# Performance work log

Measured on AMD Instinct MI355X. Metric: run time of the kernel, lower is better.

## Reference

```python
import jax, jax.numpy as jnp
import numpy as np

GAMMAK = 1.0 / 256.0  # 1/(2*d) so kernel values don't underflow for unit-gaussian data


def setup_inputs() -> dict:
    key = jax.random.key(0)
    k1, k2, k3, k4, k5 = jax.random.split(key, 5)
    N, d = 8192, 128
    X = jax.random.normal(k1, (N, d), dtype=jnp.float32)
    y = jax.random.normal(k2, (N - 1, d), dtype=jnp.float32)
    y_next = jax.random.normal(k3, (N - 1, d), dtype=jnp.float32)
    # reset_transform initializes R=eye, t=0; perturb slightly for nontrivial math
    R = jnp.eye(d, dtype=jnp.float32) + 0.01 * jax.random.normal(k4, (d, d), dtype=jnp.float32)
    t = 0.01 * jax.random.normal(k5, (d, 1), dtype=jnp.float32)
    return {"X": X, "y": y, "y_next": y_next, "R": R, "t": t}


def reference(X, y, y_next, R, t):
    # _transform_pts: (R @ y.T + t).T == y @ R.T + t.squeeze()
    yt = y @ R.T + t[:, 0]            # (N-1, d)
    Xb = X[:-1]                        # (N-1, d) kernel base points
    # pairwise_sqeuclidean(Xb, yt), clamped at 0
    sq = jnp.clip(
        jnp.sum(Xb * Xb, axis=1)[:, None]
        + jnp.sum(yt * yt, axis=1)[None, :]
        - 2.0 * (Xb @ yt.T),
        0.0, None,
    )                                  # (N-1, N-1)
    G = jnp.exp(-GAMMAK * sq)
    # diag(1/rowsum) @ G  ==  G / rowsum[:, None]  (avoids explicit NxN diagonal)
    y_pred = (G / jnp.sum(G, axis=1, keepdims=True)) @ X[1:]  # (N-1, d)
    return y_pred
```

## Files before the change

kernel.cpp:

```cpp
#include <hip/hip_runtime.h>


#define LOG2E 1.44269504088896340736f
#define KNEG (-(1.0f/256.0f)*LOG2E)
#define KA2C (2.0f*(1.0f/256.0f)*LOG2E)

typedef __attribute__((ext_vector_type(4)))  float f32x4;
typedef __attribute__((ext_vector_type(16))) float f32x16;
typedef __attribute__((ext_vector_type(8)))  short bf16x8;
typedef __attribute__((ext_vector_type(4)))  short bf16x4;

#if __has_builtin(__builtin_amdgcn_mfma_f32_32x32x8bf16_1k)
#define PV_DIRECT 1
#else
#define PV_DIRECT 0
#endif

__device__ __forceinline__ unsigned short f2bf(float f) {
  unsigned u = __builtin_bit_cast(unsigned, f);
  u = (u + 0x7fffu + ((u >> 16) & 1u)) >> 16;
  return (unsigned short)u;
}
__device__ __forceinline__ unsigned pk2bf(float a, float b) {
  return (unsigned)f2bf(a) | ((unsigned)f2bf(b) << 16);
}
__device__ __forceinline__ float fast_exp2(float x) {
#if __has_builtin(__builtin_amdgcn_exp2f)
  return __builtin_amdgcn_exp2f(x);
#else
  return exp2f(x);
#endif
}
__device__ __forceinline__ void gl2lds16(const void* g, void* l) {
  __builtin_amdgcn_global_load_lds((const __attribute__((address_space(1))) unsigned int*)g,
                                   (__attribute__((address_space(3))) unsigned int*)l, 16, 0, 0);
}
__device__ __forceinline__ void gl2lds4(const void* g, void* l) {
  __builtin_amdgcn_global_load_lds((const __attribute__((address_space(1))) unsigned int*)g,
                                   (__attribute__((address_space(3))) unsigned int*)l, 4, 0, 0);
}
__device__ __forceinline__ f32x16 mfma_32x32x16(bf16x8 a, bf16x8 b, f32x16 c) {
  return __builtin_amdgcn_mfma_f32_32x32x16_bf16(a, b, c, 0, 0, 0);
}
#if PV_DIRECT
__device__ __forceinline__ f32x16 mfma_32x32x8(bf16x4 a, bf16x4 b, f32x16 c) {
  return __builtin_amdgcn_mfma_f32_32x32x8bf16_1k(a, b, c, 0, 0, 0);
}
#endif

__global__ __launch_bounds__(128) void k_yt(const float* __restrict__ y,
                                            const float* __restrict__ R,
                                            const float* __restrict__ t,
                                            unsigned short* __restrict__ ytp,
                                            float* __restrict__ ynp) {
  __shared__ unsigned short ytt[64 * 132];
  const int tid = threadIdx.x;
  const int wv = tid >> 6;
  const int ln = tid & 63;
  const int l = ln & 31, h = ln >> 5;
  const int T = blockIdx.x;
  const int rw = T * 64 + wv * 32;

  bf16x8 af[8];
  {
    int row = rw + l; if (row > 8190) row = 8190;
    const float* yr = y + (size_t)row * 128;
#pragma unroll
    for (int kc = 0; kc < 8; ++kc) {
      float4 p0 = *(const float4*)(yr + kc*16 + 8*h);
      float4 p1 = *(const float4*)(yr + kc*16 + 8*h + 4);
      bf16x8 v;
      v[0]=(short)f2bf(p0.x); v[1]=(short)f2bf(p0.y); v[2]=(short)f2bf(p0.z); v[3]=(short)f2bf(p0.w);
      v[4]=(short)f2bf(p1.x); v[5]=(short)f2bf(p1.y); v[6]=(short)f2bf(p1.z); v[7]=(short)f2bf(p1.w);
      af[kc] = v;
    }
  }
  f32x16 acc[4];
#pragma unroll
  for (int cc=0; cc<4; ++cc)
#pragma unroll
    for (int i=0;i<16;++i) acc[cc][i] = 0.f;
#pragma unroll
  for (int cc=0; cc<4; ++cc) {
    const float* Rr = R + (size_t)(cc*32 + l) * 128;
#pragma unroll
    for (int kc=0; kc<8; ++kc) {
      float4 p0 = *(const float4*)(Rr + kc*16 + 8*h);
      float4 p1 = *(const float4*)(Rr + kc*16 + 8*h + 4);
      bf16x8 b;
      b[0]=(short)f2bf(p0.x); b[1]=(short)f2bf(p0.y); b[2]=(short)f2bf(p0.z); b[3]=(short)f2bf(p0.w);
      b[4]=(short)f2bf(p1.x); b[5]=(short)f2bf(p1.y); b[6]=(short)f2bf(p1.z); b[7]=(short)f2bf(p1.w);
      acc[cc] = mfma_32x32x16(af[kc], b, acc[cc]);
    }
  }
  float tv0 = t[l], tv1 = t[32+l], tv2 = t[64+l], tv3 = t[96+l];
  float v0[16], v1[16], v2[16], v3[16], ssq[16];
#pragma unroll
  for (int r=0;r<16;++r) {
    v0[r]=acc[0][r]+tv0; v1[r]=acc[1][r]+tv1; v2[r]=acc[2][r]+tv2; v3[r]=acc[3][r]+tv3;
    ssq[r] = v0[r]*v0[r] + v1[r]*v1[r] + v2[r]*v2[r] + v3[r]*v3[r];
  }
#pragma unroll
  for (int off=1; off<32; off<<=1)
#pragma unroll
    for (int r=0;r<16;++r) ssq[r] += __shfl_xor(ssq[r], off, 64);
  if (l < 16) {
    int r = l;
    int row = rw + (r&3) + 8*(r>>2) + 4*h;
    float val = KNEG * ssq[r];
    if (row >= 8191) val = -1e30f;
    ynp[row] = val;
  }
#pragma unroll
  for (int r=0;r<16;++r) {
    int rloc = wv*32 + (r&3) + 8*(r>>2) + 4*h;
    ytt[rloc*132 +   0 + l] = f2bf(v0[r]);
    ytt[rloc*132 +  32 + l] = f2bf(v1[r]);
    ytt[rloc*132 +  64 + l] = f2bf(v2[r]);
    ytt[rloc*132 +  96 + l] = f2bf(v3[r]);
  }
  __syncthreads();
#pragma unroll
  for (int kc=0;kc<8;++kc) {
    const unsigned short* s = &ytt[(wv*32 + l)*132 + kc*16 + 8*h];
    uint2 a = *(const uint2*)(s);
    uint2 b = *(const uint2*)(s + 4);
    uint4 o; o.x=a.x; o.y=a.y; o.z=b.x; o.w=b.y;
    *(uint4*)(ytp + (size_t)T*8192 + wv*4096 + kc*512 + ln*8) = o;
  }
}

__global__ __launch_bounds__(256) void k_x(const float* __restrict__ X,
                                           unsigned short* __restrict__ x1tp,
                                           float* __restrict__ xnp) {
  __shared__ float xt[65 * 132];
  __shared__ float ps[64][4];
  const int tid = threadIdx.x;
  const int T = blockIdx.x;
  const int jt = T * 64;
  {
    int rr = tid >> 2, q4 = tid & 3;
    int row = jt + rr; if (row > 8191) row = 8191;
    const float* src = X + (size_t)row*128 + q4*32;
    float* dst = &xt[rr*132 + q4*32];
    float s = 0.f;
#pragma unroll
    for (int i=0;i<8;++i) {
      float4 p = *(const float4*)(src + i*4);
      s += p.x*p.x + p.y*p.y + p.z*p.z + p.w*p.w;
      *(float4*)(dst + i*4) = p;
    }
    ps[rr][q4] = s;
    if (tid < 4) {
      int row2 = jt + 64; if (row2 > 8191) row2 = 8191;
      const float* s2 = X + (size_t)row2*128 + tid*32;
      float* d2 = &xt[64*132 + tid*32];
#pragma unroll
      for (int i=0;i<8;++i) *(float4*)(d2 + i*4) = *(const float4*)(s2 + i*4);
    }
  }
  __syncthreads();
  if (tid < 64) xnp[jt + tid] = KNEG * (ps[tid][0] + ps[tid][1] + ps[tid][2] + ps[tid][3]);
#if PV_DIRECT
#pragma unroll
  for (int it=0; it<8; ++it) {
    int E = tid + it*256;
    int lp = E & 63, grp = E >> 6;
    int cc = grp & 3, s = (grp >> 2) & 3, jc = grp >> 4;
    int jb = jc*32 + s*8 + 4*(lp>>5);
    int c  = cc*32 + (lp & 31);
    uint2 o;
    o.x = pk2bf(xt[(jb+1)*132 + c], xt[(jb+2)*132 + c]);
    o.y = pk2bf(xt[(jb+3)*132 + c], xt[(jb+4)*132 + c]);
    *(uint2*)(x1tp + (size_t)T*8192 + E*4) = o;
  }
#else
#pragma unroll
  for (int it=0; it<4; ++it) {
    int E = tid + it*256;
    int lp = E & 63, grp = E >> 6;
    int cc = grp & 3, jc16 = grp >> 2;
    int jb = jc16*16 + 8*(lp>>5);
    int c  = cc*32 + (lp & 31);
    uint4 o;
    o.x = pk2bf(xt[(jb+1)*132 + c], xt[(jb+2)*132 + c]);
    o.y = pk2bf(xt[(jb+3)*132 + c], xt[(jb+4)*132 + c]);
    o.z = pk2bf(xt[(jb+5)*132 + c], xt[(jb+6)*132 + c]);
    o.w = pk2bf(xt[(jb+7)*132 + c], xt[(jb+8)*132 + c]);
    *(uint4*)(x1tp + (size_t)T*8192 + E*8) = o;
  }
#endif
}

__global__ __launch_bounds__(256, 2) void k_main(
    const float* __restrict__ X,
    const unsigned short* __restrict__ ytp,
    const unsigned short* __restrict__ x1tp,
    const float* __restrict__ xnp,
    const float* __restrict__ ynp,
    float* __restrict__ accp,
    float* __restrict__ rsp,
    int tps) {
  __shared__ unsigned short yts[8192];
  __shared__ unsigned short vts[8192];
  __shared__ float yns[64];
#if !PV_DIRECT
  __shared__ unsigned short gls[4*32*68];
#endif
  const int tid = threadIdx.x;
  const int wv = tid >> 6, ln = tid & 63;
  const int l = ln & 31, h = ln >> 5;
  const int row = blockIdx.x*128 + wv*32 + l;

  bf16x8 qf[8];
  {
    const float* xr = X + (size_t)row * 128;
#pragma unroll
    for (int kc=0;kc<8;++kc) {
      float4 p0 = *(const float4*)(xr + kc*16 + 8*h);
      float4 p1 = *(const float4*)(xr + kc*16 + 8*h + 4);
      bf16x8 v;
      v[0]=(short)f2bf(p0.x); v[1]=(short)f2bf(p0.y); v[2]=(short)f2bf(p0.z); v[3]=(short)f2bf(p0.w);
      v[4]=(short)f2bf(p1.x); v[5]=(short)f2bf(p1.y); v[6]=(short)f2bf(p1.z); v[7]=(short)f2bf(p1.w);
      qf[kc]=v;
    }
  }
  const float xnl = xnp[row];
  f32x16 acc[4];
#pragma unroll
  for (int cc=0;cc<4;++cc)
#pragma unroll
    for (int i=0;i<16;++i) acc[cc][i]=0.f;
  float rs = 0.f;
  const int T0 = blockIdx.y * tps;
  for (int T = T0; T < T0 + tps; ++T) {
    __syncthreads();
    {
      const char* yb = (const char*)(ytp + (size_t)T*8192);
      const char* vb = (const char*)(x1tp + (size_t)T*8192);
#pragma unroll
      for (int i=0;i<4;++i) {
        int off = (wv*4 + i) * 1024;
        gl2lds16(yb + off + ln*16, (char*)yts + off);
        gl2lds16(vb + off + ln*16, (char*)vts + off);
      }
      if (wv == 0) gl2lds4(ynp + T*64 + ln, (char*)yns);
    }
    __syncthreads();
#pragma unroll
    for (int jc=0; jc<2; ++jc) {
      f32x16 sa;
#pragma unroll
      for (int i=0;i<16;++i) sa[i]=0.f;
#pragma unroll
      for (int kc=0;kc<8;++kc) {
        bf16x8 a = *(const bf16x8*)((const char*)yts + (jc*8+kc)*1024 + ln*16);
        sa = mfma_32x32x16(a, qf[kc], sa);
      }
      float gg[16];
#pragma unroll
      for (int rg=0; rg<4; ++rg) {
        f32x4 yv = *(const f32x4*)((const char*)yns + (jc*32 + rg*8 + 4*h)*4);
#pragma unroll
        for (int i=0;i<4;++i) {
          float e = fmaf(sa[rg*4+i], KA2C, xnl + yv[i]);
          e = fminf(e, 0.f);
          float g = fast_exp2(e);
          gg[rg*4+i] = g;
          rs += g;
        }
      }
#if PV_DIRECT
      bf16x4 pf[4];
#pragma unroll
      for (int s=0;s<4;++s) {
        bf16x4 p;
        p[0]=(short)f2bf(gg[4*s+0]); p[1]=(short)f2bf(gg[4*s+1]);
        p[2]=(short)f2bf(gg[4*s+2]); p[3]=(short)f2bf(gg[4*s+3]);
        pf[s]=p;
      }
#pragma unroll
      for (int s=0;s<4;++s)
#pragma unroll
        for (int cc=0;cc<4;++cc) {
          bf16x4 a = *(const bf16x4*)((const char*)vts + ((jc*16 + s*4 + cc)*512) + ln*8);
          acc[cc] = mfma_32x32x8(a, pf[s], acc[cc]);
        }
#else
#pragma unroll
      for (int p=0;p<8;++p) {
        int j0 = jc*32 + 2*(p&1) + 8*(p>>1) + 4*h;
        *(unsigned*)&gls[(wv*32 + l)*68 + j0] = pk2bf(gg[2*p], gg[2*p+1]);
      }
      __builtin_amdgcn_wave_barrier();
#pragma unroll
      for (int jj=0; jj<2; ++jj) {
        int jc16 = jc*2 + jj;
        const unsigned short* gp = &gls[(wv*32 + l)*68 + jc16*16 + 8*h];
        uint2 g0 = *(const uint2*)(gp);
        uint2 g1 = *(const uint2*)(gp + 4);
        uint4 gv; gv.x=g0.x; gv.y=g0.y; gv.z=g1.x; gv.w=g1.y;
        bf16x8 pb = __builtin_bit_cast(bf16x8, gv);
#pragma unroll
        for (int cc=0;cc<4;++cc) {
          bf16x8 a2 = *(const bf16x8*)((const char*)vts + (jc16*4+cc)*1024 + ln*16);
          acc[cc] = mfma_32x32x16(a2, pb, acc[cc]);
        }
      }
      __builtin_amdgcn_wave_barrier();
#endif
    }
  }
  rs += __shfl_xor(rs, 32, 64);
  const int sp = blockIdx.y;
  if (h == 0) rsp[(size_t)sp*8192 + row] = rs;
#pragma unroll
  for (int cc=0;cc<4;++cc)
#pragma unroll
    for (int r=0;r<16;++r) {
      int c = cc*32 + (r&3) + 8*(r>>2) + 4*h;
      accp[((size_t)sp*128 + c)*8192 + row] = acc[cc][r];
    }
}

__global__ __launch_bounds__(256) void k_fin(const float* __restrict__ accp,
                                             const float* __restrict__ rsp,
                                             float* __restrict__ out,
                                             int js) {
  __shared__ float tr[64*132];
  __shared__ float rinv[64];
  const int tid = threadIdx.x;
  const int r0 = blockIdx.x * 64;
  if (tid < 64) {
    float s = 0.f;
    for (int sp=0; sp<js; ++sp) s += rsp[(size_t)sp*8192 + r0 + tid];
    rinv[tid] = 1.f / s;
  }
  const int c = tid >> 1, half = tid & 1;
  float v[32];
#pragma unroll
  for (int i=0;i<32;++i) v[i]=0.f;
  for (int sp=0; sp<js; ++sp) {
    const float* src = accp + ((size_t)sp*128 + c)*8192 + r0 + half*32;
#pragma unroll
    for (int i=0;i<8;++i) {
      float4 p = *(const float4*)(src + i*4);
      v[4*i+0]+=p.x; v[4*i+1]+=p.y; v[4*i+2]+=p.z; v[4*i+3]+=p.w;
    }
  }
  __syncthreads();
#pragma unroll
  for (int i=0;i<32;++i) tr[(half*32+i)*132 + c] = v[i] * rinv[half*32+i];
  __syncthreads();
  {
    int r = tid >> 2, q = tid & 3;
    int grow = r0 + r;
    if (grow < 8191) {
      float* dst = out + (size_t)grow*128 + q*32;
      const float* s2 = &tr[r*132 + q*32];
#pragma unroll
      for (int i=0;i<8;++i) *(float4*)(dst + i*4) = *(const float4*)(s2 + i*4);
    }
  }
}

extern "C" void kernel_launch(void* const* d_in, const int* in_sizes, int n_in,
                              void* d_out, int out_size, void* d_ws, size_t ws_size,
                              hipStream_t stream) {
  const float* X = (const float*)d_in[0];
  const float* y = (const float*)d_in[1];
  const float* R = (const float*)d_in[3];
  const float* t = (const float*)d_in[4];
  float* out = (float*)d_out;
  char* ws = (char*)d_ws;

  unsigned short* ytp  = (unsigned short*)(ws);
  unsigned short* x1tp = (unsigned short*)(ws + (size_t)8192*128*2);
  float* ynp = (float*)(ws + (size_t)4*1024*1024);
  float* xnp = (float*)(ws + (size_t)4*1024*1024 + 32*1024);
  float* rsp = (float*)(ws + (size_t)4*1024*1024 + 64*1024);
  size_t accoff = (size_t)4*1024*1024 + 64*1024 + 256*1024;
  float* accp = (float*)(ws + accoff);

  int js = 8;
  while (js > 1 && accoff + (size_t)js*128*8192*4 > ws_size) js >>= 1;
  int tps = 128 / js;

  k_yt<<<dim3(128), dim3(128), 0, stream>>>(y, R, t, ytp, ynp);
  k_x<<<dim3(128), dim3(256), 0, stream>>>(X, x1tp, xnp);
  k_main<<<dim3(64, js), dim3(256), 0, stream>>>(X, ytp, x1tp, xnp, ynp, accp, rsp, tps);
  k_fin<<<dim3(128), dim3(256), 0, stream>>>(accp, rsp, out, js);
}
```

Before: 149.6 us.

## Merge prep kernels, double split-K factor, raise occupancy, retile final reduction

```diff
diff --git a/kernel.cpp b/kernel.cpp
--- a/kernel.cpp
+++ b/kernel.cpp
@@ -23,6 +23,12 @@
 }
 __device__ __forceinline__ unsigned pk2bf(float a, float b) {
   return (unsigned)f2bf(a) | ((unsigned)f2bf(b) << 16);
+}
+__device__ __forceinline__ bf16x8 pack8(float4 p0, float4 p1) {
+  uint4 u;
+  u.x = pk2bf(p0.x, p0.y); u.y = pk2bf(p0.z, p0.w);
+  u.z = pk2bf(p1.x, p1.y); u.w = pk2bf(p1.z, p1.w);
+  return __builtin_bit_cast(bf16x8, u);
 }
 __device__ __forceinline__ float fast_exp2(float x) {
 #if __has_builtin(__builtin_amdgcn_exp2f)
@@ -48,151 +54,149 @@
 }
 #endif
 
-__global__ __launch_bounds__(128) void k_yt(const float* __restrict__ y,
-                                            const float* __restrict__ R,
-                                            const float* __restrict__ t,
-                                            unsigned short* __restrict__ ytp,
-                                            float* __restrict__ ynp) {
-  __shared__ unsigned short ytt[64 * 132];
+__global__ __launch_bounds__(256) void k_prep(const float* __restrict__ y,
+                                              const float* __restrict__ R,
+                                              const float* __restrict__ t,
+                                              const float* __restrict__ X,
+                                              unsigned short* __restrict__ ytp,
+                                              float* __restrict__ ynp,
+                                              unsigned short* __restrict__ x1tp,
+                                              float* __restrict__ xnp) {
+  __shared__ union {
+    unsigned short ytt[128 * 132];
+    struct { float xt[65 * 132]; float ps[64][4]; } xb;
+  } sm;
   const int tid = threadIdx.x;
-  const int wv = tid >> 6;
-  const int ln = tid & 63;
-  const int l = ln & 31, h = ln >> 5;
-  const int T = blockIdx.x;
-  const int rw = T * 64 + wv * 32;
-
-  bf16x8 af[8];
-  {
-    int row = rw + l; if (row > 8190) row = 8190;
-    const float* yr = y + (size_t)row * 128;
-#pragma unroll
-    for (int kc = 0; kc < 8; ++kc) {
-      float4 p0 = *(const float4*)(yr + kc*16 + 8*h);
-      float4 p1 = *(const float4*)(yr + kc*16 + 8*h + 4);
-      bf16x8 v;
-      v[0]=(short)f2bf(p0.x); v[1]=(short)f2bf(p0.y); v[2]=(short)f2bf(p0.z); v[3]=(short)f2bf(p0.w);
-      v[4]=(short)f2bf(p1.x); v[5]=(short)f2bf(p1.y); v[6]=(short)f2bf(p1.z); v[7]=(short)f2bf(p1.w);
-      af[kc] = v;
-    }
-  }
-  f32x16 acc[4];
-#pragma unroll
-  for (int cc=0; cc<4; ++cc)
-#pragma unroll
-    for (int i=0;i<16;++i) acc[cc][i] = 0.f;
-#pragma unroll
-  for (int cc=0; cc<4; ++cc) {
-    const float* Rr = R + (size_t)(cc*32 + l) * 128;
-#pragma unroll
-    for (int kc=0; kc<8; ++kc) {
-      float4 p0 = *(const float4*)(Rr + kc*16 + 8*h);
-      float4 p1 = *(const float4*)(Rr + kc*16 + 8*h + 4);
-      bf16x8 b;
-      b[0]=(short)f2bf(p0.x); b[1]=(short)f2bf(p0.y); b[2]=(short)f2bf(p0.z); b[3]=(short)f2bf(p0.w);
-      b[4]=(short)f2bf(p1.x); b[5]=(short)f2bf(p1.y); b[6]=(short)f2bf(p1.z); b[7]=(short)f2bf(p1.w);
-      acc[cc] = mfma_32x32x16(af[kc], b, acc[cc]);
-    }
-  }
-  float tv0 = t[l], tv1 = t[32+l], tv2 = t[64+l], tv3 = t[96+l];
-  float v0[16], v1[16], v2[16], v3[16], ssq[16];
-#pragma unroll
-  for (int r=0;r<16;++r) {
-    v0[r]=acc[0][r]+tv0; v1[r]=acc[1][r]+tv1; v2[r]=acc[2][r]+tv2; v3[r]=acc[3][r]+tv3;
-    ssq[r] = v0[r]*v0[r] + v1[r]*v1[r] + v2[r]*v2[r] + v3[r]*v3[r];
-  }
-#pragma unroll
-  for (int off=1; off<32; off<<=1)
-#pragma unroll
-    for (int r=0;r<16;++r) ssq[r] += __shfl_xor(ssq[r], off, 64);
-  if (l < 16) {
-    int r = l;
-    int row = rw + (r&3) + 8*(r>>2) + 4*h;
-    float val = KNEG * ssq[r];
-    if (row >= 8191) val = -1e30f;
-    ynp[row] = val;
-  }
-#pragma unroll
-  for (int r=0;r<16;++r) {
-    int rloc = wv*32 + (r&3) + 8*(r>>2) + 4*h;
-    ytt[rloc*132 +   0 + l] = f2bf(v0[r]);
-    ytt[rloc*132 +  32 + l] = f2bf(v1[r]);
-    ytt[rloc*132 +  64 + l] = f2bf(v2[r]);
-    ytt[rloc*132 +  96 + l] = f2bf(v3[r]);
-  }
-  __syncthreads();
-#pragma unroll
-  for (int kc=0;kc<8;++kc) {
-    const unsigned short* s = &ytt[(wv*32 + l)*132 + kc*16 + 8*h];
-    uint2 a = *(const uint2*)(s);
-    uint2 b = *(const uint2*)(s + 4);
-    uint4 o; o.x=a.x; o.y=a.y; o.z=b.x; o.w=b.y;
-    *(uint4*)(ytp + (size_t)T*8192 + wv*4096 + kc*512 + ln*8) = o;
-  }
-}
-
-__global__ __launch_bounds__(256) void k_x(const float* __restrict__ X,
-                                           unsigned short* __restrict__ x1tp,
-                                           float* __restrict__ xnp) {
-  __shared__ float xt[65 * 132];
-  __shared__ float ps[64][4];
-  const int tid = threadIdx.x;
-  const int T = blockIdx.x;
-  const int jt = T * 64;
-  {
-    int rr = tid >> 2, q4 = tid & 3;
-    int row = jt + rr; if (row > 8191) row = 8191;
-    const float* src = X + (size_t)row*128 + q4*32;
-    float* dst = &xt[rr*132 + q4*32];
-    float s = 0.f;
-#pragma unroll
-    for (int i=0;i<8;++i) {
-      float4 p = *(const float4*)(src + i*4);
-      s += p.x*p.x + p.y*p.y + p.z*p.z + p.w*p.w;
-      *(float4*)(dst + i*4) = p;
-    }
-    ps[rr][q4] = s;
-    if (tid < 4) {
-      int row2 = jt + 64; if (row2 > 8191) row2 = 8191;
-      const float* s2 = X + (size_t)row2*128 + tid*32;
-      float* d2 = &xt[64*132 + tid*32];
-#pragma unroll
-      for (int i=0;i<8;++i) *(float4*)(d2 + i*4) = *(const float4*)(s2 + i*4);
-    }
-  }
-  __syncthreads();
-  if (tid < 64) xnp[jt + tid] = KNEG * (ps[tid][0] + ps[tid][1] + ps[tid][2] + ps[tid][3]);
+
+  if (blockIdx.x < 64) {
+    const int wv = tid >> 6, ln = tid & 63;
+    const int l = ln & 31, h = ln >> 5;
+    const int B = blockIdx.x;
+    const int rw = B * 128 + wv * 32;
+
+    bf16x8 af[8];
+    {
+      int row = rw + l; if (row > 8190) row = 8190;
+      const float* yr = y + (size_t)row * 128;
+#pragma unroll
+      for (int kc = 0; kc < 8; ++kc) {
+        float4 p0 = *(const float4*)(yr + kc*16 + 8*h);
+        float4 p1 = *(const float4*)(yr + kc*16 + 8*h + 4);
+        af[kc] = pack8(p0, p1);
+      }
+    }
+    f32x16 acc[4];
+#pragma unroll
+    for (int cc=0; cc<4; ++cc)
+#pragma unroll
+      for (int i=0;i<16;++i) acc[cc][i] = 0.f;
+#pragma unroll
+    for (int cc=0; cc<4; ++cc) {
+      const float* Rr = R + (size_t)(cc*32 + l) * 128;
+#pragma unroll
+      for (int kc=0; kc<8; ++kc) {
+        float4 p0 = *(const float4*)(Rr + kc*16 + 8*h);
+        float4 p1 = *(const float4*)(Rr + kc*16 + 8*h + 4);
+        acc[cc] = mfma_32x32x16(af[kc], pack8(p0, p1), acc[cc]);
+      }
+    }
+    float tv0 = t[l], tv1 = t[32+l], tv2 = t[64+l], tv3 = t[96+l];
+    float v0[16], v1[16], v2[16], v3[16], ssq[16];
+#pragma unroll
+    for (int r=0;r<16;++r) {
+      v0[r]=acc[0][r]+tv0; v1[r]=acc[1][r]+tv1; v2[r]=acc[2][r]+tv2; v3[r]=acc[3][r]+tv3;
+      ssq[r] = v0[r]*v0[r] + v1[r]*v1[r] + v2[r]*v2[r] + v3[r]*v3[r];
+    }
+#pragma unroll
+    for (int off=1; off<32; off<<=1)
+#pragma unroll
+      for (int r=0;r<16;++r) ssq[r] += __shfl_xor(ssq[r], off, 64);
+    if (l < 16) {
+      int r = l;
+      int row = rw + (r&3) + 8*(r>>2) + 4*h;
+      float val = KNEG * ssq[r];
+      if (row >= 8191) val = -1e30f;
+      ynp[row] = val;
+    }
+#pragma unroll
+    for (int r=0;r<16;++r) {
+      int rloc = wv*32 + (r&3) + 8*(r>>2) + 4*h;
+      sm.ytt[rloc*132 +   0 + l] = f2bf(v0[r]);
+      sm.ytt[rloc*132 +  32 + l] = f2bf(v1[r]);
+      sm.ytt[rloc*132 +  64 + l] = f2bf(v2[r]);
+      sm.ytt[rloc*132 +  96 + l] = f2bf(v3[r]);
+    }
+    __syncthreads();
+    const int Tt = B*2 + (wv>>1);
+    const int jcw = wv & 1;
+#pragma unroll
+    for (int kc=0;kc<8;++kc) {
+      const unsigned short* s = &sm.ytt[(wv*32 + l)*132 + kc*16 + 8*h];
+      uint2 a = *(const uint2*)(s);
+      uint2 b = *(const uint2*)(s + 4);
+      uint4 o; o.x=a.x; o.y=a.y; o.z=b.x; o.w=b.y;
+      *(uint4*)(ytp + (size_t)Tt*8192 + jcw*4096 + kc*512 + ln*8) = o;
+    }
+  } else {
+    const int T = blockIdx.x - 64;
+    const int jt = T * 64;
+    {
+      int rr = tid >> 2, q4 = tid & 3;
+      int row = jt + rr; if (row > 8191) row = 8191;
+      const float* src = X + (size_t)row*128 + q4*32;
+      float* dst = &sm.xb.xt[rr*132 + q4*32];
+      float s = 0.f;
+#pragma unroll
+      for (int i=0;i<8;++i) {
+        float4 p = *(const float4*)(src + i*4);
+        s += p.x*p.x + p.y*p.y + p.z*p.z + p.w*p.w;
+        *(float4*)(dst + i*4) = p;
+      }
+      sm.xb.ps[rr][q4] = s;
+      if (tid < 4) {
+        int row2 = jt + 64; if (row2 > 8191) row2 = 8191;
+        const float* s2 = X + (size_t)row2*128 + tid*32;
+        float* d2 = &sm.xb.xt[64*132 + tid*32];
+#pragma unroll
+        for (int i=0;i<8;++i) *(float4*)(d2 + i*4) = *(const float4*)(s2 + i*4);
+      }
+    }
+    __syncthreads();
+    if (tid < 64) xnp[jt + tid] = KNEG * (sm.xb.ps[tid][0] + sm.xb.ps[tid][1] +
+                                          sm.xb.ps[tid][2] + sm.xb.ps[tid][3]);
 #if PV_DIRECT
 #pragma unroll
-  for (int it=0; it<8; ++it) {
-    int E = tid + it*256;
-    int lp = E & 63, grp = E >> 6;
-    int cc = grp & 3, s = (grp >> 2) & 3, jc = grp >> 4;
-    int jb = jc*32 + s*8 + 4*(lp>>5);
-    int c  = cc*32 + (lp & 31);
-    uint2 o;
-    o.x = pk2bf(xt[(jb+1)*132 + c], xt[(jb+2)*132 + c]);
-    o.y = pk2bf(xt[(jb+3)*132 + c], xt[(jb+4)*132 + c]);
-    *(uint2*)(x1tp + (size_t)T*8192 + E*4) = o;
-  }
+    for (int it=0; it<8; ++it) {
+      int E = tid + it*256;
+      int lp = E & 63, grp = E >> 6;
+      int cc = grp & 3, s = (grp >> 2) & 3, jc = grp >> 4;
+      int jb = jc*32 + s*8 + 4*(lp>>5);
+      int c  = cc*32 + (lp & 31);
+      uint2 o;
+      o.x = pk2bf(sm.xb.xt[(jb+1)*132 + c], sm.xb.xt[(jb+2)*132 + c]);
+      o.y = pk2bf(sm.xb.xt[(jb+3)*132 + c], sm.xb.xt[(jb+4)*132 + c]);
+      *(uint2*)(x1tp + (size_t)T*8192 + E*4) = o;
+    }
 #else
 #pragma unroll
-  for (int it=0; it<4; ++it) {
-    int E = tid + it*256;
-    int lp = E & 63, grp = E >> 6;
-    int cc = grp & 3, jc16 = grp >> 2;
-    int jb = jc16*16 + 8*(lp>>5);
-    int c  = cc*32 + (lp & 31);
-    uint4 o;
-    o.x = pk2bf(xt[(jb+1)*132 + c], xt[(jb+2)*132 + c]);
-    o.y = pk2bf(xt[(jb+3)*132 + c], xt[(jb+4)*132 + c]);
-    o.z = pk2bf(xt[(jb+5)*132 + c], xt[(jb+6)*132 + c]);
-    o.w = pk2bf(xt[(jb+7)*132 + c], xt[(jb+8)*132 + c]);
-    *(uint4*)(x1tp + (size_t)T*8192 + E*8) = o;
-  }
-#endif
-}
-
-__global__ __launch_bounds__(256, 2) void k_main(
+    for (int it=0; it<4; ++it) {
+      int E = tid + it*256;
+      int lp = E & 63, grp = E >> 6;
+      int cc = grp & 3, jc16 = grp >> 2;
+      int jb = jc16*16 + 8*(lp>>5);
+      int c  = cc*32 + (lp & 31);
+      uint4 o;
+      o.x = pk2bf(sm.xb.xt[(jb+1)*132 + c], sm.xb.xt[(jb+2)*132 + c]);
+      o.y = pk2bf(sm.xb.xt[(jb+3)*132 + c], sm.xb.xt[(jb+4)*132 + c]);
+      o.z = pk2bf(sm.xb.xt[(jb+5)*132 + c], sm.xb.xt[(jb+6)*132 + c]);
+      o.w = pk2bf(sm.xb.xt[(jb+7)*132 + c], sm.xb.xt[(jb+8)*132 + c]);
+      *(uint4*)(x1tp + (size_t)T*8192 + E*8) = o;
+    }
+#endif
+  }
+}
+
+__global__ __launch_bounds__(256, 4) void k_main(
     const float* __restrict__ X,
     const unsigned short* __restrict__ ytp,
     const unsigned short* __restrict__ x1tp,
@@ -219,10 +223,7 @@
     for (int kc=0;kc<8;++kc) {
       float4 p0 = *(const float4*)(xr + kc*16 + 8*h);
       float4 p1 = *(const float4*)(xr + kc*16 + 8*h + 4);
-      bf16x8 v;
-      v[0]=(short)f2bf(p0.x); v[1]=(short)f2bf(p0.y); v[2]=(short)f2bf(p0.z); v[3]=(short)f2bf(p0.w);
-      v[4]=(short)f2bf(p1.x); v[5]=(short)f2bf(p1.y); v[6]=(short)f2bf(p1.z); v[7]=(short)f2bf(p1.w);
-      qf[kc]=v;
+      qf[kc] = pack8(p0, p1);
     }
   }
   const float xnl = xnp[row];
@@ -274,10 +275,10 @@
       bf16x4 pf[4];
 #pragma unroll
       for (int s=0;s<4;++s) {
-        bf16x4 p;
-        p[0]=(short)f2bf(gg[4*s+0]); p[1]=(short)f2bf(gg[4*s+1]);
-        p[2]=(short)f2bf(gg[4*s+2]); p[3]=(short)f2bf(gg[4*s+3]);
-        pf[s]=p;
+        uint2 u;
+        u.x = pk2bf(gg[4*s+0], gg[4*s+1]);
+        u.y = pk2bf(gg[4*s+2], gg[4*s+3]);
+        pf[s] = __builtin_bit_cast(bf16x4, u);
       }
 #pragma unroll
       for (int s=0;s<4;++s)
@@ -336,21 +337,26 @@
     for (int sp=0; sp<js; ++sp) s += rsp[(size_t)sp*8192 + r0 + tid];
     rinv[tid] = 1.f / s;
   }
-  const int c = tid >> 1, half = tid & 1;
-  float v[32];
-#pragma unroll
-  for (int i=0;i<32;++i) v[i]=0.f;
+  const int rq = tid & 15, cg = tid >> 4;
+  float v[8][4];
+#pragma unroll
+  for (int cc=0;cc<8;++cc)
+#pragma unroll
+    for (int k=0;k<4;++k) v[cc][k]=0.f;
   for (int sp=0; sp<js; ++sp) {
-    const float* src = accp + ((size_t)sp*128 + c)*8192 + r0 + half*32;
-#pragma unroll
-    for (int i=0;i<8;++i) {
-      float4 p = *(const float4*)(src + i*4);
-      v[4*i+0]+=p.x; v[4*i+1]+=p.y; v[4*i+2]+=p.z; v[4*i+3]+=p.w;
+    const float* base = accp + ((size_t)sp*128 + cg*8)*8192 + r0 + rq*4;
+#pragma unroll
+    for (int cc=0; cc<8; ++cc) {
+      float4 p = *(const float4*)(base + (size_t)cc*8192);
+      v[cc][0]+=p.x; v[cc][1]+=p.y; v[cc][2]+=p.z; v[cc][3]+=p.w;
     }
   }
   __syncthreads();
 #pragma unroll
-  for (int i=0;i<32;++i) tr[(half*32+i)*132 + c] = v[i] * rinv[half*32+i];
+  for (int cc=0;cc<8;++cc)
+#pragma unroll
+    for (int k=0;k<4;++k)
+      tr[(rq*4+k)*132 + cg*8+cc] = v[cc][k] * rinv[rq*4+k];
   __syncthreads();
   {
     int r = tid >> 2, q = tid & 3;
@@ -379,15 +385,14 @@
   float* ynp = (float*)(ws + (size_t)4*1024*1024);
   float* xnp = (float*)(ws + (size_t)4*1024*1024 + 32*1024);
   float* rsp = (float*)(ws + (size_t)4*1024*1024 + 64*1024);
-  size_t accoff = (size_t)4*1024*1024 + 64*1024 + 256*1024;
+  size_t accoff = (size_t)4*1024*1024 + 64*1024 + 512*1024;
   float* accp = (float*)(ws + accoff);
 
-  int js = 8;
+  int js = 16;
   while (js > 1 && accoff + (size_t)js*128*8192*4 > ws_size) js >>= 1;
   int tps = 128 / js;
 
-  k_yt<<<dim3(128), dim3(128), 0, stream>>>(y, R, t, ytp, ynp);
-  k_x<<<dim3(128), dim3(256), 0, stream>>>(X, x1tp, xnp);
+  k_prep<<<dim3(192), dim3(256), 0, stream>>>(y, R, t, X, ytp, ynp, x1tp, xnp);
   k_main<<<dim3(64, js), dim3(256), 0, stream>>>(X, ytp, x1tp, xnp, ynp, accp, rsp, tps);
   k_fin<<<dim3(128), dim3(256), 0, stream>>>(accp, rsp, out, js);
 }
```

New measurement: 179.6 us. 20.1% more time.
